# Kernel tuning notes

Measured on AMD Instinct MI355X. Metric: run time of the kernel, lower is better.

Reference implementation:

```python
import math
import jax, jax.numpy as jnp
import numpy as np

N_HEADS = 8
D_MODEL = 512
HEAD_DIM = D_MODEL // N_HEADS
N, S = 4, 2048


def setup_inputs() -> dict:
    key = jax.random.key(0)
    ks = jax.random.split(key, 9)
    inp = {
        "value": jax.random.normal(ks[0], (N, S, D_MODEL), dtype=jnp.float32),
        "key": jax.random.normal(ks[1], (N, S, D_MODEL), dtype=jnp.float32),
        "query": jax.random.normal(ks[2], (N, S, D_MODEL), dtype=jnp.float32),
        "mask": jax.random.randint(ks[3], (N, 1, 1, S), 0, 2, dtype=jnp.int32),
        # nn.Linear weights: [out, in]; projections are head_dim x head_dim, shared across heads
        "Wv": jax.random.normal(ks[4], (HEAD_DIM, HEAD_DIM), dtype=jnp.float32) / math.sqrt(HEAD_DIM),
        "Wk": jax.random.normal(ks[5], (HEAD_DIM, HEAD_DIM), dtype=jnp.float32) / math.sqrt(HEAD_DIM),
        "Wq": jax.random.normal(ks[6], (HEAD_DIM, HEAD_DIM), dtype=jnp.float32) / math.sqrt(HEAD_DIM),
        "Wfc": jax.random.normal(ks[7], (D_MODEL, D_MODEL), dtype=jnp.float32) / math.sqrt(D_MODEL),
        "bfc": jax.random.normal(ks[8], (D_MODEL,), dtype=jnp.float32) * 0.01,
    }
    return inp


def reference(value, key, query, mask, Wv, Wk, Wq, Wfc, bfc):
    n = query.shape[0]
    sv, sk, sq = value.shape[1], key.shape[1], query.shape[1]
    # split heads: [N, S, H, D]
    v = value.reshape(n, sv, N_HEADS, HEAD_DIM) @ Wv.T
    k = key.reshape(n, sk, N_HEADS, HEAD_DIM) @ Wk.T
    q = query.reshape(n, sq, N_HEADS, HEAD_DIM) @ Wq.T
    # [N, H, Q, K] scores
    scores = jnp.einsum('nqhd,nkhd->nhqk', q, k)
    scores = jnp.where(mask == 0, jnp.float32(-1e20), scores)
    # NOTE: original divides by sqrt(head_dim) AFTER the masked_fill; kept faithful
    attn = jax.nn.softmax(scores / math.sqrt(HEAD_DIM), axis=3)
    out = jnp.einsum('nhqk,nkhd->nqhd', attn, v).reshape(n, sq, D_MODEL)
    return out @ Wfc.T + bfc
```

## Files before the change

kernel.cpp:

```cpp
#include <hip/hip_runtime.h>

#define N_B 4
#define SEQ 2048
#define NH 8
#define HD 64
#define DM 512

typedef __attribute__((ext_vector_type(8))) short bf16x8;
typedef __attribute__((ext_vector_type(4))) short bf16x4;
typedef __attribute__((ext_vector_type(4))) float f32x4;

__device__ __forceinline__ unsigned short f2b(float f) {
  unsigned int u = __float_as_uint(f);
  u += 0x7FFFu + ((u >> 16) & 1u);
  return (unsigned short)(u >> 16);
}
__device__ __forceinline__ float b2f(unsigned short s) {
  return __uint_as_float(((unsigned int)s) << 16);
}
__device__ __forceinline__ unsigned int pack2(float a, float b) {
  return (unsigned int)f2b(a) | ((unsigned int)f2b(b) << 16);
}
__device__ __forceinline__ f32x4 mfma32(bf16x8 a, bf16x8 b, f32x4 c) {
  return __builtin_amdgcn_mfma_f32_16x16x32_bf16(a, b, c, 0, 0, 0);
}
__device__ __forceinline__ f32x4 mfma16k(bf16x4 a, bf16x4 b, f32x4 c) {
  return __builtin_amdgcn_mfma_f32_16x16x16bf16_1k(a, b, c, 0, 0, 0);
}
__device__ __forceinline__ bf16x8 cvt8(const float* p) {
  float4 x = *(const float4*)p;
  float4 y = *(const float4*)(p + 4);
  union { unsigned int u[4]; bf16x8 v; } r;
  r.u[0] = pack2(x.x, x.y); r.u[1] = pack2(x.z, x.w);
  r.u[2] = pack2(y.x, y.y); r.u[3] = pack2(y.z, y.w);
  return r.v;
}

__global__ __launch_bounds__(256, 4) void proj_kernel(
    const float* __restrict__ qin, const float* __restrict__ kin, const float* __restrict__ vin,
    const float* __restrict__ Wq, const float* __restrict__ Wk, const float* __restrict__ Wv,
    unsigned short* __restrict__ Qp, unsigned short* __restrict__ Kp, unsigned short* __restrict__ Vp)
{
  __shared__ __align__(16) unsigned short Wl[64][72];
  const int tid = threadIdx.x, lane = tid & 63, w = tid >> 6;
  const int hi = lane >> 4, lo = lane & 15;
  const int z = blockIdx.z, nh = blockIdx.y, n = nh >> 3, h = nh & 7;
  const float* W = z == 0 ? Wq : (z == 1 ? Wk : Wv);
  const int srow = tid >> 2, scol = (tid & 3) * 16;
  *(bf16x8*)&Wl[srow][scol]     = cvt8(&W[srow * 64 + scol]);
  *(bf16x8*)&Wl[srow][scol + 8] = cvt8(&W[srow * 64 + scol + 8]);
  __syncthreads();

  const float* in = z == 0 ? qin : (z == 1 ? kin : vin);
  const int sx = blockIdx.x * 64 + w * 16 + lo;
  const float* src = in + ((size_t)(n * SEQ + sx)) * DM + h * HD + hi * 8;
  bf16x8 a0 = cvt8(src), a1 = cvt8(src + 32);

  f32x4 acc[4];
  #pragma unroll
  for (int t = 0; t < 4; ++t) acc[t] = (f32x4){0.f, 0.f, 0.f, 0.f};
  bf16x8 wf0[4], wf1[4];
  #pragma unroll
  for (int t = 0; t < 4; ++t) {
    wf0[t] = *(const bf16x8*)&Wl[t * 16 + lo][hi * 8];
    wf1[t] = *(const bf16x8*)&Wl[t * 16 + lo][32 + hi * 8];
  }
  if (z < 2) {
    #pragma unroll
    for (int t = 0; t < 4; ++t) {
      acc[t] = mfma32(wf0[t], a0, acc[t]);
      acc[t] = mfma32(wf1[t], a1, acc[t]);
    }
    unsigned short* outp = z == 0 ? Qp : Kp;
    unsigned short* dst = outp + ((size_t)(nh * SEQ + sx)) * HD + hi * 4;
    #pragma unroll
    for (int t = 0; t < 4; ++t) {
      uint2 u; u.x = pack2(acc[t][0], acc[t][1]); u.y = pack2(acc[t][2], acc[t][3]);
      *(uint2*)(dst + t * 16) = u;
    }
  } else {
    #pragma unroll
    for (int t = 0; t < 4; ++t) {
      acc[t] = mfma32(a0, wf0[t], acc[t]);
      acc[t] = mfma32(a1, wf1[t], acc[t]);
    }
    const int rbase = blockIdx.x * 64 + w * 16 + hi * 4;
    #pragma unroll
    for (int t = 0; t < 4; ++t) {
      uint2 u; u.x = pack2(acc[t][0], acc[t][1]); u.y = pack2(acc[t][2], acc[t][3]);
      *(uint2*)&Vp[((size_t)(nh * HD + t * 16 + lo)) * SEQ + rbase] = u;
    }
  }
}

__global__ __launch_bounds__(256, 2) void attn_kernel(
    const unsigned short* __restrict__ Qp, const unsigned short* __restrict__ Kp,
    const unsigned short* __restrict__ Vp, const int* __restrict__ mask,
    unsigned short* __restrict__ AO)
{
  __shared__ __align__(16) unsigned short Kl[64][72];
  __shared__ __align__(16) unsigned short Vt[64][72];
  __shared__ float maskf[64];

  const int tid = threadIdx.x, lane = tid & 63, w = tid >> 6;
  const int hi = lane >> 4, lo = lane & 15;
  const int nh = blockIdx.y, n = nh >> 3, h = nh & 7;
  const int qb = blockIdx.x * 128 + w * 32;
  const float CS = 0.18033688011112042f;

  bf16x8 qa[2][2];
  #pragma unroll
  for (int qs = 0; qs < 2; ++qs) {
    const unsigned short* qsrc = Qp + ((size_t)(nh * SEQ + qb + qs * 16 + lo)) * HD + hi * 8;
    qa[qs][0] = *(const bf16x8*)qsrc;
    qa[qs][1] = *(const bf16x8*)(qsrc + 32);
  }

  f32x4 o[2][4];
  #pragma unroll
  for (int qs = 0; qs < 2; ++qs)
    #pragma unroll
    for (int dt = 0; dt < 4; ++dt) o[qs][dt] = (f32x4){0.f, 0.f, 0.f, 0.f};
  float m[2] = {-1e30f, -1e30f}, l[2] = {0.f, 0.f};

  const int srow = tid >> 2, scol = (tid & 3) * 16;
  const unsigned short* Kb = Kp + ((size_t)(nh * SEQ + srow)) * HD + scol;
  const unsigned short* Vb = Vp + ((size_t)(nh * HD + srow)) * SEQ + scol;
  const int* Mb = mask + n * SEQ;

  for (int kv = 0; kv < SEQ / 64; ++kv) {
    const int kb = kv * 64;
    __syncthreads();
    *(int4*)&Kl[srow][scol]     = *(const int4*)(Kb + (size_t)kb * HD);
    *(int4*)&Kl[srow][scol + 8] = *(const int4*)(Kb + (size_t)kb * HD + 8);
    *(int4*)&Vt[srow][scol]     = *(const int4*)(Vb + kb);
    *(int4*)&Vt[srow][scol + 8] = *(const int4*)(Vb + kb + 8);
    if (tid < 64) maskf[tid] = Mb[kb + tid] ? 1.f : 0.f;
    __syncthreads();

    bf16x8 ka[4][2];
    #pragma unroll
    for (int t = 0; t < 4; ++t) {
      ka[t][0] = *(const bf16x8*)&Kl[t * 16 + lo][hi * 8];
      ka[t][1] = *(const bf16x8*)&Kl[t * 16 + lo][32 + hi * 8];
    }
    bf16x4 va[4][4];
    #pragma unroll
    for (int dt = 0; dt < 4; ++dt)
      #pragma unroll
      for (int t = 0; t < 4; ++t)
        va[dt][t] = *(const bf16x4*)&Vt[dt * 16 + lo][t * 16 + hi * 4];
    f32x4 mb[4];
    #pragma unroll
    for (int t = 0; t < 4; ++t) mb[t] = *(const f32x4*)&maskf[t * 16 + hi * 4];

    #pragma unroll
    for (int qs = 0; qs < 2; ++qs) {
      f32x4 st[4];
      #pragma unroll
      for (int t = 0; t < 4; ++t) {
        st[t] = mfma32(ka[t][0], qa[qs][0], (f32x4){0.f, 0.f, 0.f, 0.f});
        st[t] = mfma32(ka[t][1], qa[qs][1], st[t]);
      }
      f32x4 mx;
      #pragma unroll
      for (int j = 0; j < 4; ++j)
        mx[j] = fmaxf(fmaxf(st[0][j], st[1][j]), fmaxf(st[2][j], st[3][j]));
      float mxx = fmaxf(fmaxf(mx[0], mx[1]), fmaxf(mx[2], mx[3]));
      mxx = fmaxf(mxx, __shfl_xor(mxx, 16));
      mxx = fmaxf(mxx, __shfl_xor(mxx, 32));
      const float nm = fmaxf(m[qs], mxx);
      const float sc = exp2f((m[qs] - nm) * CS);
      m[qs] = nm;
      const float mc = -nm * CS;

      bf16x4 pf[4];
      float prs = 0.f;
      #pragma unroll
      for (int t = 0; t < 4; ++t) {
        union { unsigned short s[4]; bf16x4 v; } pu;
        #pragma unroll
        for (int j = 0; j < 4; ++j) {
          float p = exp2f(fmaf(st[t][j], CS, mc)) * mb[t][j];
          unsigned short us = f2b(p);
          pu.s[j] = us;
          prs += b2f(us);
        }
        pf[t] = pu.v;
      }
      prs += __shfl_xor(prs, 16);
      prs += __shfl_xor(prs, 32);
      l[qs] = l[qs] * sc + prs;
      #pragma unroll
      for (int dt = 0; dt < 4; ++dt) o[qs][dt] *= sc;
      #pragma unroll
      for (int dt = 0; dt < 4; ++dt)
        #pragma unroll
        for (int t = 0; t < 4; ++t)
          o[qs][dt] = mfma16k(va[dt][t], pf[t], o[qs][dt]);
    }
  }

  #pragma unroll
  for (int qs = 0; qs < 2; ++qs) {
    const float rl = 1.f / l[qs];
    unsigned short* dst = AO + ((size_t)(n * SEQ + qb + qs * 16 + lo)) * DM + h * HD + hi * 4;
    #pragma unroll
    for (int dt = 0; dt < 4; ++dt) {
      f32x4 v = o[qs][dt] * rl;
      uint2 u; u.x = pack2(v[0], v[1]); u.y = pack2(v[2], v[3]);
      *(uint2*)(dst + dt * 16) = u;
    }
  }
}

__global__ __launch_bounds__(256, 4) void fc_kernel(
    const unsigned short* __restrict__ AO, const float* __restrict__ Wfc,
    const float* __restrict__ bfc, float* __restrict__ out)
{
  __shared__ __align__(16) unsigned short Al[64][72];
  __shared__ __align__(16) unsigned short Bl[64][72];
  const int tid = threadIdx.x, lane = tid & 63, w = tid >> 6;
  const int hi = lane >> 4, lo = lane & 15;
  const int rb = blockIdx.x * 64, cb = blockIdx.y * 64;
  const int srow = tid >> 2, scol = (tid & 3) * 16;
  const unsigned short* Ab = AO + (size_t)(rb + srow) * DM + scol;
  const float* Bb = Wfc + (size_t)(cb + srow) * DM + scol;

  f32x4 acc[4];
  #pragma unroll
  for (int t = 0; t < 4; ++t) acc[t] = (f32x4){0.f, 0.f, 0.f, 0.f};

  for (int i = 0; i < 8; ++i) {
    const int kn = i * 64;
    __syncthreads();
    *(int4*)&Al[srow][scol]      = *(const int4*)(Ab + kn);
    *(int4*)&Al[srow][scol + 8]  = *(const int4*)(Ab + kn + 8);
    *(bf16x8*)&Bl[srow][scol]     = cvt8(Bb + kn);
    *(bf16x8*)&Bl[srow][scol + 8] = cvt8(Bb + kn + 8);
    __syncthreads();

    bf16x8 a0 = *(const bf16x8*)&Al[w * 16 + lo][hi * 8];
    bf16x8 a1 = *(const bf16x8*)&Al[w * 16 + lo][32 + hi * 8];
    #pragma unroll
    for (int t = 0; t < 4; ++t) {
      bf16x8 w0 = *(const bf16x8*)&Bl[t * 16 + lo][hi * 8];
      bf16x8 w1 = *(const bf16x8*)&Bl[t * 16 + lo][32 + hi * 8];
      acc[t] = mfma32(w0, a0, acc[t]);
      acc[t] = mfma32(w1, a1, acc[t]);
    }
  }

  const int orow = rb + w * 16 + lo;
  float* dst = out + (size_t)orow * DM + cb + hi * 4;
  #pragma unroll
  for (int t = 0; t < 4; ++t) {
    float4 b4 = *(const float4*)&bfc[cb + t * 16 + hi * 4];
    float4 v;
    v.x = acc[t][0] + b4.x; v.y = acc[t][1] + b4.y;
    v.z = acc[t][2] + b4.z; v.w = acc[t][3] + b4.w;
    *(float4*)(dst + t * 16) = v;
  }
}

extern "C" void kernel_launch(void* const* d_in, const int* in_sizes, int n_in,
                              void* d_out, int out_size, void* d_ws, size_t ws_size,
                              hipStream_t stream) {
  const float* value = (const float*)d_in[0];
  const float* key   = (const float*)d_in[1];
  const float* query = (const float*)d_in[2];
  const int*   mask  = (const int*)d_in[3];
  const float* Wv    = (const float*)d_in[4];
  const float* Wk    = (const float*)d_in[5];
  const float* Wq    = (const float*)d_in[6];
  const float* Wfc   = (const float*)d_in[7];
  const float* bfc   = (const float*)d_in[8];
  float* out = (float*)d_out;

  const size_t per = (size_t)N_B * NH * SEQ * HD;
  unsigned short* Qp = (unsigned short*)d_ws;
  unsigned short* Kp = Qp + per;
  unsigned short* Vp = Kp + per;
  unsigned short* AO = Vp + per;

  proj_kernel<<<dim3(SEQ / 64, N_B * NH, 3), 256, 0, stream>>>(
      query, key, value, Wq, Wk, Wv, Qp, Kp, Vp);
  attn_kernel<<<dim3(SEQ / 128, N_B * NH), 256, 0, stream>>>(Qp, Kp, Vp, mask, AO);
  fc_kernel<<<dim3(N_B * SEQ / 64, DM / 64), 256, 0, stream>>>(AO, Wfc, bfc, out);
}
```

Baseline: 222.8 us.

## Prefetch tiles into registers, add lazy softmax rescale, use native bf16 conversion

Attention and FC kernels now load the next K/V/mask (or A/W) tile into registers while the current tile is being stored to LDS, which overlaps global loads with compute. The softmax skips the running-max rescale unless the new max exceeds the old one by a threshold, and uses the hardware exp2 builtin. Manual bf16 rounding is replaced by the HIP intrinsic. V fragments are read with wider LDS loads. Projection and FC operand order changes, giving different output store patterns, some of them scalar stores that may coalesce worse.

```diff
diff --git a/kernel.cpp b/kernel.cpp
--- a/kernel.cpp
+++ b/kernel.cpp
@@ -1,4 +1,5 @@
 #include <hip/hip_runtime.h>
+#include <hip/hip_bf16.h>
 
 #define N_B 4
 #define SEQ 2048
@@ -10,16 +11,14 @@
 typedef __attribute__((ext_vector_type(4))) short bf16x4;
 typedef __attribute__((ext_vector_type(4))) float f32x4;
 
-__device__ __forceinline__ unsigned short f2b(float f) {
-  unsigned int u = __float_as_uint(f);
-  u += 0x7FFFu + ((u >> 16) & 1u);
-  return (unsigned short)(u >> 16);
-}
-__device__ __forceinline__ float b2f(unsigned short s) {
-  return __uint_as_float(((unsigned int)s) << 16);
-}
-__device__ __forceinline__ unsigned int pack2(float a, float b) {
-  return (unsigned int)f2b(a) | ((unsigned int)f2b(b) << 16);
+#if __has_builtin(__builtin_amdgcn_exp2f)
+#define EXP2(x) __builtin_amdgcn_exp2f(x)
+#else
+#define EXP2(x) exp2f(x)
+#endif
+
+__device__ __forceinline__ unsigned short b16(float f) {
+  return __bfloat16_as_ushort(__float2bfloat16(f));
 }
 __device__ __forceinline__ f32x4 mfma32(bf16x8 a, bf16x8 b, f32x4 c) {
   return __builtin_amdgcn_mfma_f32_16x16x32_bf16(a, b, c, 0, 0, 0);
@@ -30,9 +29,15 @@
 __device__ __forceinline__ bf16x8 cvt8(const float* p) {
   float4 x = *(const float4*)p;
   float4 y = *(const float4*)(p + 4);
-  union { unsigned int u[4]; bf16x8 v; } r;
-  r.u[0] = pack2(x.x, x.y); r.u[1] = pack2(x.z, x.w);
-  r.u[2] = pack2(y.x, y.y); r.u[3] = pack2(y.z, y.w);
+  union { unsigned short s[8]; bf16x8 v; } r;
+  r.s[0] = b16(x.x); r.s[1] = b16(x.y); r.s[2] = b16(x.z); r.s[3] = b16(x.w);
+  r.s[4] = b16(y.x); r.s[5] = b16(y.y); r.s[6] = b16(y.z); r.s[7] = b16(y.w);
+  return r.v;
+}
+__device__ __forceinline__ bf16x8 cvt8v(float4 x, float4 y) {
+  union { unsigned short s[8]; bf16x8 v; } r;
+  r.s[0] = b16(x.x); r.s[1] = b16(x.y); r.s[2] = b16(x.z); r.s[3] = b16(x.w);
+  r.s[4] = b16(y.x); r.s[5] = b16(y.y); r.s[6] = b16(y.z); r.s[7] = b16(y.w);
   return r.v;
 }
 
@@ -59,36 +64,30 @@
   f32x4 acc[4];
   #pragma unroll
   for (int t = 0; t < 4; ++t) acc[t] = (f32x4){0.f, 0.f, 0.f, 0.f};
-  bf16x8 wf0[4], wf1[4];
   #pragma unroll
   for (int t = 0; t < 4; ++t) {
-    wf0[t] = *(const bf16x8*)&Wl[t * 16 + lo][hi * 8];
-    wf1[t] = *(const bf16x8*)&Wl[t * 16 + lo][32 + hi * 8];
-  }
+    bf16x8 wf0 = *(const bf16x8*)&Wl[t * 16 + lo][hi * 8];
+    bf16x8 wf1 = *(const bf16x8*)&Wl[t * 16 + lo][32 + hi * 8];
+    acc[t] = mfma32(a0, wf0, acc[t]);
+    acc[t] = mfma32(a1, wf1, acc[t]);
+  }
+
   if (z < 2) {
+    unsigned short* outp = z == 0 ? Qp : Kp;
+    const size_t rowb = (size_t)(nh * SEQ + blockIdx.x * 64 + w * 16 + hi * 4);
+    #pragma unroll
+    for (int t = 0; t < 4; ++t)
+      #pragma unroll
+      for (int j = 0; j < 4; ++j)
+        outp[(rowb + j) * HD + t * 16 + lo] = b16(acc[t][j]);
+  } else {
+    const int cb = blockIdx.x * 64 + hi * 16 + w * 4;
     #pragma unroll
     for (int t = 0; t < 4; ++t) {
-      acc[t] = mfma32(wf0[t], a0, acc[t]);
-      acc[t] = mfma32(wf1[t], a1, acc[t]);
-    }
-    unsigned short* outp = z == 0 ? Qp : Kp;
-    unsigned short* dst = outp + ((size_t)(nh * SEQ + sx)) * HD + hi * 4;
-    #pragma unroll
-    for (int t = 0; t < 4; ++t) {
-      uint2 u; u.x = pack2(acc[t][0], acc[t][1]); u.y = pack2(acc[t][2], acc[t][3]);
-      *(uint2*)(dst + t * 16) = u;
-    }
-  } else {
-    #pragma unroll
-    for (int t = 0; t < 4; ++t) {
-      acc[t] = mfma32(a0, wf0[t], acc[t]);
-      acc[t] = mfma32(a1, wf1[t], acc[t]);
-    }
-    const int rbase = blockIdx.x * 64 + w * 16 + hi * 4;
-    #pragma unroll
-    for (int t = 0; t < 4; ++t) {
-      uint2 u; u.x = pack2(acc[t][0], acc[t][1]); u.y = pack2(acc[t][2], acc[t][3]);
-      *(uint2*)&Vp[((size_t)(nh * HD + t * 16 + lo)) * SEQ + rbase] = u;
+      union { unsigned short s[4]; uint2 u; } p;
+      p.s[0] = b16(acc[t][0]); p.s[1] = b16(acc[t][1]);
+      p.s[2] = b16(acc[t][2]); p.s[3] = b16(acc[t][3]);
+      *(uint2*)&Vp[((size_t)(nh * HD + t * 16 + lo)) * SEQ + cb] = p.u;
     }
   }
 }
@@ -107,6 +106,7 @@
   const int nh = blockIdx.y, n = nh >> 3, h = nh & 7;
   const int qb = blockIdx.x * 128 + w * 32;
   const float CS = 0.18033688011112042f;
+  const float THR = 44.0f;
 
   bf16x8 qa[2][2];
   #pragma unroll
@@ -128,14 +128,23 @@
   const unsigned short* Vb = Vp + ((size_t)(nh * HD + srow)) * SEQ + scol;
   const int* Mb = mask + n * SEQ;
 
+  int4 kr0 = *(const int4*)Kb, kr1 = *(const int4*)(Kb + 8);
+  int4 vr0 = *(const int4*)Vb, vr1 = *(const int4*)(Vb + 8);
+  int mp = (tid < 64) ? Mb[tid] : 0;
+
   for (int kv = 0; kv < SEQ / 64; ++kv) {
-    const int kb = kv * 64;
     __syncthreads();
-    *(int4*)&Kl[srow][scol]     = *(const int4*)(Kb + (size_t)kb * HD);
-    *(int4*)&Kl[srow][scol + 8] = *(const int4*)(Kb + (size_t)kb * HD + 8);
-    *(int4*)&Vt[srow][scol]     = *(const int4*)(Vb + kb);
-    *(int4*)&Vt[srow][scol + 8] = *(const int4*)(Vb + kb + 8);
-    if (tid < 64) maskf[tid] = Mb[kb + tid] ? 1.f : 0.f;
+    *(int4*)&Kl[srow][scol] = kr0; *(int4*)&Kl[srow][scol + 8] = kr1;
+    *(int4*)&Vt[srow][scol] = vr0; *(int4*)&Vt[srow][scol + 8] = vr1;
+    if (tid < 64) maskf[tid] = mp ? 1.f : 0.f;
+    {
+      const int kb2 = ((kv + 1) & 31) * 64;
+      kr0 = *(const int4*)(Kb + (size_t)kb2 * HD);
+      kr1 = *(const int4*)(Kb + (size_t)kb2 * HD + 8);
+      vr0 = *(const int4*)(Vb + kb2);
+      vr1 = *(const int4*)(Vb + kb2 + 8);
+      if (tid < 64) mp = Mb[kb2 + tid];
+    }
     __syncthreads();
 
     bf16x8 ka[4][2];
@@ -144,12 +153,13 @@
       ka[t][0] = *(const bf16x8*)&Kl[t * 16 + lo][hi * 8];
       ka[t][1] = *(const bf16x8*)&Kl[t * 16 + lo][32 + hi * 8];
     }
-    bf16x4 va[4][4];
-    #pragma unroll
-    for (int dt = 0; dt < 4; ++dt)
-      #pragma unroll
-      for (int t = 0; t < 4; ++t)
-        va[dt][t] = *(const bf16x4*)&Vt[dt * 16 + lo][t * 16 + hi * 4];
+    union V16 { bf16x8 v8[2]; bf16x4 v4[4]; };
+    V16 vv[4];
+    #pragma unroll
+    for (int dt = 0; dt < 4; ++dt) {
+      vv[dt].v8[0] = *(const bf16x8*)&Vt[dt * 16 + lo][hi * 16];
+      vv[dt].v8[1] = *(const bf16x8*)&Vt[dt * 16 + lo][hi * 16 + 8];
+    }
     f32x4 mb[4];
     #pragma unroll
     for (int t = 0; t < 4; ++t) mb[t] = *(const f32x4*)&maskf[t * 16 + hi * 4];
@@ -169,35 +179,41 @@
       float mxx = fmaxf(fmaxf(mx[0], mx[1]), fmaxf(mx[2], mx[3]));
       mxx = fmaxf(mxx, __shfl_xor(mxx, 16));
       mxx = fmaxf(mxx, __shfl_xor(mxx, 32));
-      const float nm = fmaxf(m[qs], mxx);
-      const float sc = exp2f((m[qs] - nm) * CS);
-      m[qs] = nm;
-      const float mc = -nm * CS;
+      if (!__all(mxx - m[qs] <= THR)) {
+        const float nm = fmaxf(m[qs], mxx);
+        const float sc = EXP2((m[qs] - nm) * CS);
+        m[qs] = nm;
+        l[qs] *= sc;
+        #pragma unroll
+        for (int dt = 0; dt < 4; ++dt) o[qs][dt] *= sc;
+      }
+      const float mc = -m[qs] * CS;
+
+      f32x4 pv[4];
+      #pragma unroll
+      for (int t = 0; t < 4; ++t)
+        #pragma unroll
+        for (int j = 0; j < 4; ++j)
+          pv[t][j] = EXP2(fmaf(st[t][j], CS, mc)) * mb[t][j];
+      f32x4 ps = pv[0] + pv[1] + pv[2] + pv[3];
+      float prs = ps[0] + ps[1] + ps[2] + ps[3];
+      prs += __shfl_xor(prs, 16);
+      prs += __shfl_xor(prs, 32);
+      l[qs] += prs;
 
       bf16x4 pf[4];
-      float prs = 0.f;
       #pragma unroll
       for (int t = 0; t < 4; ++t) {
         union { unsigned short s[4]; bf16x4 v; } pu;
-        #pragma unroll
-        for (int j = 0; j < 4; ++j) {
-          float p = exp2f(fmaf(st[t][j], CS, mc)) * mb[t][j];
-          unsigned short us = f2b(p);
-          pu.s[j] = us;
-          prs += b2f(us);
-        }
+        pu.s[0] = b16(pv[t][0]); pu.s[1] = b16(pv[t][1]);
+        pu.s[2] = b16(pv[t][2]); pu.s[3] = b16(pv[t][3]);
         pf[t] = pu.v;
       }
-      prs += __shfl_xor(prs, 16);
-      prs += __shfl_xor(prs, 32);
-      l[qs] = l[qs] * sc + prs;
-      #pragma unroll
-      for (int dt = 0; dt < 4; ++dt) o[qs][dt] *= sc;
       #pragma unroll
       for (int dt = 0; dt < 4; ++dt)
         #pragma unroll
         for (int t = 0; t < 4; ++t)
-          o[qs][dt] = mfma16k(va[dt][t], pf[t], o[qs][dt]);
+          o[qs][dt] = mfma16k(vv[dt].v4[t], pf[t], o[qs][dt]);
     }
   }
 
@@ -208,8 +224,9 @@
     #pragma unroll
     for (int dt = 0; dt < 4; ++dt) {
       f32x4 v = o[qs][dt] * rl;
-      uint2 u; u.x = pack2(v[0], v[1]); u.y = pack2(v[2], v[3]);
-      *(uint2*)(dst + dt * 16) = u;
+      union { unsigned short s[4]; uint2 u; } p;
+      p.s[0] = b16(v[0]); p.s[1] = b16(v[1]); p.s[2] = b16(v[2]); p.s[3] = b16(v[3]);
+      *(uint2*)(dst + dt * 16) = p.u;
     }
   }
 }
@@ -227,17 +244,25 @@
   const unsigned short* Ab = AO + (size_t)(rb + srow) * DM + scol;
   const float* Bb = Wfc + (size_t)(cb + srow) * DM + scol;
 
+  int4 ar0 = *(const int4*)Ab, ar1 = *(const int4*)(Ab + 8);
+  float4 wr0 = *(const float4*)Bb,        wr1 = *(const float4*)(Bb + 4);
+  float4 wr2 = *(const float4*)(Bb + 8),  wr3 = *(const float4*)(Bb + 12);
+
   f32x4 acc[4];
   #pragma unroll
   for (int t = 0; t < 4; ++t) acc[t] = (f32x4){0.f, 0.f, 0.f, 0.f};
 
   for (int i = 0; i < 8; ++i) {
-    const int kn = i * 64;
     __syncthreads();
-    *(int4*)&Al[srow][scol]      = *(const int4*)(Ab + kn);
-    *(int4*)&Al[srow][scol + 8]  = *(const int4*)(Ab + kn + 8);
-    *(bf16x8*)&Bl[srow][scol]     = cvt8(Bb + kn);
-    *(bf16x8*)&Bl[srow][scol + 8] = cvt8(Bb + kn + 8);
+    *(int4*)&Al[srow][scol] = ar0; *(int4*)&Al[srow][scol + 8] = ar1;
+    *(bf16x8*)&Bl[srow][scol]     = cvt8v(wr0, wr1);
+    *(bf16x8*)&Bl[srow][scol + 8] = cvt8v(wr2, wr3);
+    {
+      const int kn = ((i + 1) & 7) * 64;
+      ar0 = *(const int4*)(Ab + kn); ar1 = *(const int4*)(Ab + kn + 8);
+      wr0 = *(const float4*)(Bb + kn);      wr1 = *(const float4*)(Bb + kn + 4);
+      wr2 = *(const float4*)(Bb + kn + 8);  wr3 = *(const float4*)(Bb + kn + 12);
+    }
     __syncthreads();
 
     bf16x8 a0 = *(const bf16x8*)&Al[w * 16 + lo][hi * 8];
@@ -246,20 +271,18 @@
     for (int t = 0; t < 4; ++t) {
       bf16x8 w0 = *(const bf16x8*)&Bl[t * 16 + lo][hi * 8];
       bf16x8 w1 = *(const bf16x8*)&Bl[t * 16 + lo][32 + hi * 8];
-      acc[t] = mfma32(w0, a0, acc[t]);
-      acc[t] = mfma32(w1, a1, acc[t]);
-    }
-  }
-
-  const int orow = rb + w * 16 + lo;
-  float* dst = out + (size_t)orow * DM + cb + hi * 4;
+      acc[t] = mfma32(a0, w0, acc[t]);
+      acc[t] = mfma32(a1, w1, acc[t]);
+    }
+  }
+
+  const int rowb = rb + w * 16 + hi * 4;
   #pragma unroll
   for (int t = 0; t < 4; ++t) {
-    float4 b4 = *(const float4*)&bfc[cb + t * 16 + hi * 4];
-    float4 v;
-    v.x = acc[t][0] + b4.x; v.y = acc[t][1] + b4.y;
-    v.z = acc[t][2] + b4.z; v.w = acc[t][3] + b4.w;
-    *(float4*)(dst + t * 16) = v;
+    const float bias = bfc[cb + t * 16 + lo];
+    #pragma unroll
+    for (int j = 0; j < 4; ++j)
+      out[(size_t)(rowb + j) * DM + cb + t * 16 + lo] = acc[t][j] + bias;
   }
 }
 
```

Result: faster. 197.0 us (-11.6%).
